# Kernel tuning notes

Hardware: AMD Instinct MI355X
Metric: run time of the kernel (lower is better)

Reference implementation:

```python
import jax, jax.numpy as jnp
import numpy as np

N = 100000   # nodes
E = 1600000  # edges
D = 128      # input_dim
H = 128      # hidden_dim
O = 64       # output_dim


def setup_inputs() -> dict:
    key = jax.random.key(0)
    ks = jax.random.split(key, 10)
    x = jax.random.normal(ks[0], (N, D), dtype=jnp.float32)
    edge_index = jax.random.randint(ks[1], (2, E), 0, N, dtype=jnp.int32)

    def glorot(k, fan_in, fan_out):
        lim = np.sqrt(6.0 / (fan_in + fan_out)).astype(np.float32)
        return jax.random.uniform(k, (fan_in, fan_out), jnp.float32, -lim, lim)

    return {
        "x": x,
        "edge_index": edge_index,
        "W0": glorot(ks[2], D, H), "b0": jnp.zeros((H,), jnp.float32),
        "W1": glorot(ks[3], H, H), "b1": jnp.zeros((H,), jnp.float32),
        "W2": glorot(ks[4], H, H), "b2": jnp.zeros((H,), jnp.float32),
        "W3": glorot(ks[5], H, O), "b3": jnp.zeros((O,), jnp.float32),
    }


def gcn_conv(x, src, dst, W, b):
    """PyG GCNConv: out = D^{-1/2} (A + I) D^{-1/2} (x W) + b."""
    n = x.shape[0]
    h = x @ W                                # [N, out]
    loop = jnp.arange(n, dtype=src.dtype)    # self loops
    s = jnp.concatenate([src, loop])
    d = jnp.concatenate([dst, loop])
    deg = jax.ops.segment_sum(jnp.ones_like(d, dtype=h.dtype), d, num_segments=n)
    dinv = jax.lax.rsqrt(jnp.maximum(deg, 1.0))  # deg >= 1 because of self loops
    norm = dinv[s] * dinv[d]                     # [E+N]
    out = jax.ops.segment_sum(h[s] * norm[:, None], d, num_segments=n)
    return out + b


def reference(x, edge_index, W0, b0, W1, b1, W2, b2, W3, b3):
    src, dst = edge_index[0], edge_index[1]
    # three GCNBlocks: GCNConv + ReLU (dropout disabled)
    h = jax.nn.relu(gcn_conv(x, src, dst, W0, b0))
    h = jax.nn.relu(gcn_conv(h, src, dst, W1, b1))
    h = jax.nn.relu(gcn_conv(h, src, dst, W2, b2))
    # final bare GCNConv -> output_dim (no activation)
    return gcn_conv(h, src, dst, W3, b3)
```

## Files before the change

kernel.cpp:

```cpp
#include <hip/hip_runtime.h>
#include <math.h>

#define NN 100000
#define NE 1600000
#define NB 391

typedef __attribute__((ext_vector_type(8))) short short8;
typedef __attribute__((ext_vector_type(4))) float f32x4;
union frag8 { short s[8]; short8 v; };

__device__ __forceinline__ void split_bf16(float a, short& hi, short& lo) {
    unsigned u = __float_as_uint(a);
    unsigned hb = u & 0xffff0000u;
    hi = (short)(hb >> 16);
    float r = a - __uint_as_float(hb);
    unsigned lu = __float_as_uint(r);
    lo = (short)((lu + 0x7fff + ((lu >> 16) & 1)) >> 16);
}

__global__ __launch_bounds__(256) void hist_k(const int* __restrict__ dst, int* __restrict__ hist, int e) {
    __shared__ int h[NB];
    int t = threadIdx.x;
    for (int i = t; i < NB; i += 256) h[i] = 0;
    __syncthreads();
    int base = blockIdx.x * 4096;
#pragma unroll
    for (int j = 0; j < 16; ++j) {
        int i = base + j * 256 + t;
        if (i < e) atomicAdd(&h[dst[i] >> 8], 1);
    }
    __syncthreads();
    for (int i = t; i < NB; i += 256) if (h[i]) atomicAdd(&hist[i], h[i]);
}

__global__ __launch_bounds__(512) void bktscan_k(const int* __restrict__ hist,
                                                 int* __restrict__ boff, int* __restrict__ bcur) {
    __shared__ int wsum[8];
    int t = threadIdx.x, lane = t & 63, wid = t >> 6;
    int v = (t < NB) ? hist[t] : 0;
    int inc = v;
#pragma unroll
    for (int off = 1; off < 64; off <<= 1) {
        int tt = __shfl_up(inc, off);
        if (lane >= off) inc += tt;
    }
    if (lane == 63) wsum[wid] = inc;
    __syncthreads();
    int woff = 0;
    for (int w = 0; w < wid; ++w) woff += wsum[w];
    int excl = inc - v + woff;
    if (t < NB) { boff[t] = excl; bcur[t] = excl; }
    if (t == NB - 1) boff[NB] = excl + v;
}

__global__ __launch_bounds__(256) void part2_k(const int* __restrict__ src, const int* __restrict__ dst,
                                               int* bcur, int2* __restrict__ pairs, int e) {
    __shared__ int lhist[NB];
    __shared__ int lbase[NB];
    int t = threadIdx.x;
    for (int i = t; i < NB; i += 256) lhist[i] = 0;
    __syncthreads();
    int e0 = blockIdx.x * 4096;
    int sreg[16], dreg[16];
#pragma unroll
    for (int j = 0; j < 16; ++j) {
        int i = e0 + j * 256 + t;
        if (i < e) {
            sreg[j] = src[i];
            dreg[j] = dst[i];
            atomicAdd(&lhist[dreg[j] >> 8], 1);
        } else dreg[j] = -1;
    }
    __syncthreads();
    for (int i = t; i < NB; i += 256) {
        int c = lhist[i];
        lbase[i] = c ? atomicAdd(&bcur[i], c) : 0;
        lhist[i] = 0;
    }
    __syncthreads();
#pragma unroll
    for (int j = 0; j < 16; ++j) {
        if (dreg[j] >= 0) {
            int b = dreg[j] >> 8;
            int pos = lbase[b] + atomicAdd(&lhist[b], 1);
            pairs[pos] = make_int2(sreg[j], dreg[j]);
        }
    }
}

__global__ __launch_bounds__(256) void csr_k(const int2* __restrict__ pairs, const int* __restrict__ boff,
                                             float* __restrict__ dinv, int* __restrict__ rowptr,
                                             int* __restrict__ csr_src, int n) {
    __shared__ int cnt[256];
    __shared__ int wsum[4];
    __shared__ int lcur[256];
    int b = blockIdx.x, t = threadIdx.x;
    cnt[t] = 0;
    __syncthreads();
    int e0 = boff[b], e1 = boff[b + 1];
    for (int e = e0 + t; e < e1; e += 256) atomicAdd(&cnt[pairs[e].y & 255], 1);
    __syncthreads();
    int c = cnt[t];
    int lane = t & 63, wid = t >> 6;
    int inc = c;
#pragma unroll
    for (int off = 1; off < 64; off <<= 1) {
        int tt = __shfl_up(inc, off);
        if (lane >= off) inc += tt;
    }
    if (lane == 63) wsum[wid] = inc;
    __syncthreads();
    int woff = 0;
    for (int w = 0; w < wid; ++w) woff += wsum[w];
    int excl = inc - c + woff + e0;
    int i = (b << 8) + t;
    if (i < n) {
        rowptr[i] = excl;
        dinv[i] = 1.0f / sqrtf((float)(c + 1));
    }
    if (b == NB - 1 && t == 255) rowptr[n] = e1;
    lcur[t] = excl;
    __syncthreads();
    for (int e = e0 + t; e < e1; e += 256) {
        int2 p = pairs[e];
        int pos = atomicAdd(&lcur[p.y & 255], 1);
        csr_src[pos] = p.x;
    }
}

__global__ __launch_bounds__(256) void convw_k(const float* __restrict__ W0, const float* __restrict__ W1,
                                               const float* __restrict__ W2, const float* __restrict__ W3,
                                               short* __restrict__ wt) {
    int gid = blockIdx.x * 256 + threadIdx.x;
    if (gid >= 57344) return;
    const float* W;
    int elem, Ncols, hi_base;
    if (gid < 49152) {
        int w = gid >> 14;
        elem = gid & 16383;
        Ncols = 128;
        W = (w == 0) ? W0 : (w == 1) ? W1 : W2;
        hi_base = w * 32768;
    } else {
        elem = gid - 49152;
        Ncols = 64;
        W = W3;
        hi_base = 98304;
    }
    int k = elem / Ncols, ncol = elem % Ncols;
    short hi, lo;
    split_bf16(W[elem], hi, lo);
    int dstidx = ncol * 128 + k;
    wt[hi_base + dstidx] = hi;
    wt[hi_base + Ncols * 128 + dstidx] = lo;
}

__global__ __launch_bounds__(256) void mfma_gemm_k(const float* __restrict__ A,
                                                   const short* __restrict__ wt_hi,
                                                   const short* __restrict__ wt_lo,
                                                   const float* __restrict__ dinv,
                                                   float* __restrict__ C, int n) {
    constexpr int NT = 8;
    const int tid = threadIdx.x;
    const int wid = tid >> 6, lane = tid & 63;
    const int arow = blockIdx.x * 64 + wid * 16 + (lane & 15);
    const int khalf = lane >> 4;

    f32x4 acc[NT];
#pragma unroll
    for (int nt = 0; nt < NT; ++nt) acc[nt] = (f32x4){0.f, 0.f, 0.f, 0.f};

#pragma unroll
    for (int kc = 0; kc < 4; ++kc) {
        const int k0 = kc * 32 + khalf * 8;
        float4 a0 = make_float4(0.f, 0.f, 0.f, 0.f), a1 = a0;
        if (arow < n) {
            a0 = *(const float4*)(A + (size_t)arow * 128 + k0);
            a1 = *(const float4*)(A + (size_t)arow * 128 + k0 + 4);
        }
        frag8 ahi, alo;
        float av[8] = {a0.x, a0.y, a0.z, a0.w, a1.x, a1.y, a1.z, a1.w};
#pragma unroll
        for (int j = 0; j < 8; ++j) split_bf16(av[j], ahi.s[j], alo.s[j]);

#pragma unroll
        for (int nt = 0; nt < NT; ++nt) {
            const size_t bidx = (size_t)(nt * 16 + (lane & 15)) * 128 + k0;
            short8 bhi = *(const short8*)(wt_hi + bidx);
            short8 blo = *(const short8*)(wt_lo + bidx);
            acc[nt] = __builtin_amdgcn_mfma_f32_16x16x32_bf16(alo.v, bhi, acc[nt], 0, 0, 0);
            acc[nt] = __builtin_amdgcn_mfma_f32_16x16x32_bf16(ahi.v, blo, acc[nt], 0, 0, 0);
            acc[nt] = __builtin_amdgcn_mfma_f32_16x16x32_bf16(ahi.v, bhi, acc[nt], 0, 0, 0);
        }
    }

    const int rbase = blockIdx.x * 64 + wid * 16 + khalf * 4;
    const int col = lane & 15;
    float dv[4];
#pragma unroll
    for (int r = 0; r < 4; ++r) dv[r] = (rbase + r < n) ? dinv[rbase + r] : 0.f;
#pragma unroll
    for (int nt = 0; nt < NT; ++nt) {
#pragma unroll
        for (int r = 0; r < 4; ++r) {
            int row = rbase + r;
            if (row < n) C[(size_t)row * 128 + nt * 16 + col] = acc[nt][r] * dv[r];
        }
    }
}

template<int HOUT>
__global__ __launch_bounds__(256) void fused_k(const float* __restrict__ tmp,
                                               const int* __restrict__ csr_src,
                                               const int* __restrict__ rowptr,
                                               const float* __restrict__ dinv,
                                               const float* __restrict__ bias,
                                               const short* __restrict__ wt_hi,
                                               const short* __restrict__ wt_lo,
                                               float* __restrict__ C) {
    constexpr int NT = HOUT / 32;
    __shared__ float As[32][132];
    const int t = threadIdx.x;
    const int row0 = blockIdx.x * 32;

    {
        const int l = t & 31;
        const int sub = t >> 5;
        float4 bb = *(const float4*)(bias + l * 4);
        int eptr[4], eend[4];
#pragma unroll
        for (int it = 0; it < 4; ++it) {
            int node = row0 + it * 8 + sub;
            eptr[it] = rowptr[node];
            eend[it] = rowptr[node + 1];
        }
        int pf = (eptr[0] + l < eend[0]) ? csr_src[eptr[0] + l] : 0;
#pragma unroll
        for (int it = 0; it < 4; ++it) {
            const int node = row0 + it * 8 + sub;
            const float dn = dinv[node];
            float4 acc = *(const float4*)(tmp + (size_t)node * 128 + l * 4);
            int myidx = pf;
            if (it < 3)
                pf = (eptr[it + 1] + l < eend[it + 1]) ? csr_src[eptr[it + 1] + l] : 0;
            int e = eptr[it];
            const int end = eend[it];
            while (e < end) {
                int m = end - e;
                if (m > 32) m = 32;
                int j = 0;
                for (; j + 4 <= m; j += 4) {
                    int s0 = __shfl(myidx, j, 32);
                    int s1 = __shfl(myidx, j + 1, 32);
                    int s2 = __shfl(myidx, j + 2, 32);
                    int s3 = __shfl(myidx, j + 3, 32);
                    float4 v0 = *(const float4*)(tmp + (size_t)s0 * 128 + l * 4);
                    float4 v1 = *(const float4*)(tmp + (size_t)s1 * 128 + l * 4);
                    float4 v2 = *(const float4*)(tmp + (size_t)s2 * 128 + l * 4);
                    float4 v3 = *(const float4*)(tmp + (size_t)s3 * 128 + l * 4);
                    acc.x += (v0.x + v1.x) + (v2.x + v3.x);
                    acc.y += (v0.y + v1.y) + (v2.y + v3.y);
                    acc.z += (v0.z + v1.z) + (v2.z + v3.z);
                    acc.w += (v0.w + v1.w) + (v2.w + v3.w);
                }
                for (; j < m; ++j) {
                    int s0 = __shfl(myidx, j, 32);
                    float4 v0 = *(const float4*)(tmp + (size_t)s0 * 128 + l * 4);
                    acc.x += v0.x; acc.y += v0.y; acc.z += v0.z; acc.w += v0.w;
                }
                e += m;
                if (e < end)
                    myidx = (e + l < end) ? csr_src[e + l] : 0;
            }
            acc.x = fmaxf(fmaf(acc.x, dn, bb.x), 0.f);
            acc.y = fmaxf(fmaf(acc.y, dn, bb.y), 0.f);
            acc.z = fmaxf(fmaf(acc.z, dn, bb.z), 0.f);
            acc.w = fmaxf(fmaf(acc.w, dn, bb.w), 0.f);
            *(float4*)&As[it * 8 + sub][l * 4] = acc;
        }
    }
    __syncthreads();

    const int wid = t >> 6, lane = t & 63;
    const int rt = wid & 1;
    const int cg = wid >> 1;
    const int arow_l = rt * 16 + (lane & 15);
    const int khalf = lane >> 4;

    f32x4 acc[NT];
#pragma unroll
    for (int nt = 0; nt < NT; ++nt) acc[nt] = (f32x4){0.f, 0.f, 0.f, 0.f};

#pragma unroll
    for (int kc = 0; kc < 4; ++kc) {
        const int k0 = kc * 32 + khalf * 8;
        float4 a0 = *(const float4*)&As[arow_l][k0];
        float4 a1 = *(const float4*)&As[arow_l][k0 + 4];
        frag8 ahi, alo;
        float av[8] = {a0.x, a0.y, a0.z, a0.w, a1.x, a1.y, a1.z, a1.w};
#pragma unroll
        for (int j = 0; j < 8; ++j) split_bf16(av[j], ahi.s[j], alo.s[j]);

#pragma unroll
        for (int nt = 0; nt < NT; ++nt) {
            const size_t bidx = (size_t)(cg * NT * 16 + nt * 16 + (lane & 15)) * 128 + k0;
            short8 bhi = *(const short8*)(wt_hi + bidx);
            short8 blo = *(const short8*)(wt_lo + bidx);
            acc[nt] = __builtin_amdgcn_mfma_f32_16x16x32_bf16(alo.v, bhi, acc[nt], 0, 0, 0);
            acc[nt] = __builtin_amdgcn_mfma_f32_16x16x32_bf16(ahi.v, blo, acc[nt], 0, 0, 0);
            acc[nt] = __builtin_amdgcn_mfma_f32_16x16x32_bf16(ahi.v, bhi, acc[nt], 0, 0, 0);
        }
    }

    const int rbase = row0 + rt * 16 + khalf * 4;
    const int col = lane & 15;
    float dv[4];
#pragma unroll
    for (int r = 0; r < 4; ++r) dv[r] = dinv[rbase + r];
#pragma unroll
    for (int nt = 0; nt < NT; ++nt) {
#pragma unroll
        for (int r = 0; r < 4; ++r) {
            C[(size_t)(rbase + r) * HOUT + cg * NT * 16 + nt * 16 + col] = acc[nt][r] * dv[r];
        }
    }
}

template<int HOUT>
__global__ __launch_bounds__(256) void agg2_k(const float* __restrict__ tmp,
                                              const int* __restrict__ csr_src,
                                              const int* __restrict__ rowptr,
                                              const float* __restrict__ dinv,
                                              const float* __restrict__ bias,
                                              float* __restrict__ out, int n) {
    constexpr int LPN = HOUT / 4;
    int gid = blockIdx.x * 256 + threadIdx.x;
    int node = gid / LPN, l = gid % LPN;
    if (node >= n) return;

    const float dn = dinv[node];
    float4 bb = *(const float4*)(bias + l * 4);
    float4 acc = *(const float4*)(tmp + (size_t)node * HOUT + l * 4);

    int e = rowptr[node];
    const int end = rowptr[node + 1];
    while (e < end) {
        int m = end - e;
        if (m > LPN) m = LPN;
        int myidx = (e + l < end) ? csr_src[e + l] : 0;
        int j = 0;
        for (; j + 4 <= m; j += 4) {
            int s0 = __shfl(myidx, j, LPN);
            int s1 = __shfl(myidx, j + 1, LPN);
            int s2 = __shfl(myidx, j + 2, LPN);
            int s3 = __shfl(myidx, j + 3, LPN);
            float4 v0 = *(const float4*)(tmp + (size_t)s0 * HOUT + l * 4);
            float4 v1 = *(const float4*)(tmp + (size_t)s1 * HOUT + l * 4);
            float4 v2 = *(const float4*)(tmp + (size_t)s2 * HOUT + l * 4);
            float4 v3 = *(const float4*)(tmp + (size_t)s3 * HOUT + l * 4);
            acc.x += (v0.x + v1.x) + (v2.x + v3.x);
            acc.y += (v0.y + v1.y) + (v2.y + v3.y);
            acc.z += (v0.z + v1.z) + (v2.z + v3.z);
            acc.w += (v0.w + v1.w) + (v2.w + v3.w);
        }
        for (; j < m; ++j) {
            int s0 = __shfl(myidx, j, LPN);
            float4 v0 = *(const float4*)(tmp + (size_t)s0 * HOUT + l * 4);
            acc.x += v0.x; acc.y += v0.y; acc.z += v0.z; acc.w += v0.w;
        }
        e += m;
    }
    float4 o;
    o.x = fmaf(acc.x, dn, bb.x);
    o.y = fmaf(acc.y, dn, bb.y);
    o.z = fmaf(acc.z, dn, bb.z);
    o.w = fmaf(acc.w, dn, bb.w);
    *(float4*)(out + (size_t)node * HOUT + l * 4) = o;
}

extern "C" void kernel_launch(void* const* d_in, const int* in_sizes, int n_in,
                              void* d_out, int out_size, void* d_ws, size_t ws_size,
                              hipStream_t stream) {
    const float* x    = (const float*)d_in[0];
    const int*   ei   = (const int*)d_in[1];
    const int*   srcp = ei;
    const int*   dstp = ei + NE;
    const float* W0 = (const float*)d_in[2]; const float* b0 = (const float*)d_in[3];
    const float* W1 = (const float*)d_in[4]; const float* b1 = (const float*)d_in[5];
    const float* W2 = (const float*)d_in[6]; const float* b2 = (const float*)d_in[7];
    const float* W3 = (const float*)d_in[8]; const float* b3 = (const float*)d_in[9];
    float* out = (float*)d_out;

    char* ws = (char*)d_ws;
    size_t off = 0;
    auto alloc = [&](size_t bytes) { void* p = ws + off; off = (off + bytes + 255) & ~(size_t)255; return p; };
    int*   hist    = (int*)alloc((size_t)NB * 4);
    int*   boff    = (int*)alloc((size_t)(NB + 1) * 4);
    int*   bcur    = (int*)alloc((size_t)NB * 4);
    float* dinv    = (float*)alloc((size_t)NN * 4);
    int*   rowptr  = (int*)alloc((size_t)(NN + 1) * 4);
    int*   csr_src = (int*)alloc((size_t)NE * 4);
    short* wt      = (short*)alloc((size_t)114688 * 2);
    float* bufA    = (float*)alloc((size_t)NN * 128 * 4);
    float* bufB    = (float*)alloc((size_t)NN * 128 * 4);
    int2*  pairs   = (int2*)bufA;

    const int nblk_e4k  = (NE + 4095) / 4096;
    const int nblk_g    = (NN + 63) / 64;
    const int nblk_f    = NN / 32;
    const int nblk_a64  = (int)(((size_t)NN * 16 + 255) / 256);

    hipMemsetAsync(hist, 0, (size_t)NB * 4, stream);
    hist_k<<<nblk_e4k, 256, 0, stream>>>(dstp, hist, NE);
    bktscan_k<<<1, 512, 0, stream>>>(hist, boff, bcur);
    part2_k<<<nblk_e4k, 256, 0, stream>>>(srcp, dstp, bcur, pairs, NE);
    csr_k<<<NB, 256, 0, stream>>>(pairs, boff, dinv, rowptr, csr_src, NN);
    convw_k<<<(57344 + 255) / 256, 256, 0, stream>>>(W0, W1, W2, W3, wt);

    const short* w0h = wt,          *w0l = wt + 16384;
    const short* w1h = wt + 32768,  *w1l = wt + 49152;
    const short* w2h = wt + 65536,  *w2l = wt + 81920;
    const short* w3h = wt + 98304,  *w3l = wt + 106496;

    mfma_gemm_k<<<nblk_g, 256, 0, stream>>>(x, w0h, w0l, dinv, bufB, NN);
    fused_k<128><<<nblk_f, 256, 0, stream>>>(bufB, csr_src, rowptr, dinv, b0, w1h, w1l, bufA);
    fused_k<128><<<nblk_f, 256, 0, stream>>>(bufA, csr_src, rowptr, dinv, b1, w2h, w2l, bufB);
    fused_k<64><<<nblk_f, 256, 0, stream>>>(bufB, csr_src, rowptr, dinv, b2, w3h, w3l, bufA);
    agg2_k<64><<<nblk_a64, 256, 0, stream>>>(bufA, csr_src, rowptr, dinv, b3, out, NN);
}
```

Before: 618.1 us.

## Replace histogram+scan CSR build with fixed-capacity bucket slots and row descriptors

Measured after the change: 604.8 us. 1.02x faster.

```diff
diff --git a/kernel.cpp b/kernel.cpp
--- a/kernel.cpp
+++ b/kernel.cpp
@@ -4,6 +4,7 @@
 #define NN 100000
 #define NE 1600000
 #define NB 391
+#define CAP 4608
 
 typedef __attribute__((ext_vector_type(8))) short short8;
 typedef __attribute__((ext_vector_type(4))) float f32x4;
@@ -18,41 +19,6 @@
     lo = (short)((lu + 0x7fff + ((lu >> 16) & 1)) >> 16);
 }
 
-__global__ __launch_bounds__(256) void hist_k(const int* __restrict__ dst, int* __restrict__ hist, int e) {
-    __shared__ int h[NB];
-    int t = threadIdx.x;
-    for (int i = t; i < NB; i += 256) h[i] = 0;
-    __syncthreads();
-    int base = blockIdx.x * 4096;
-#pragma unroll
-    for (int j = 0; j < 16; ++j) {
-        int i = base + j * 256 + t;
-        if (i < e) atomicAdd(&h[dst[i] >> 8], 1);
-    }
-    __syncthreads();
-    for (int i = t; i < NB; i += 256) if (h[i]) atomicAdd(&hist[i], h[i]);
-}
-
-__global__ __launch_bounds__(512) void bktscan_k(const int* __restrict__ hist,
-                                                 int* __restrict__ boff, int* __restrict__ bcur) {
-    __shared__ int wsum[8];
-    int t = threadIdx.x, lane = t & 63, wid = t >> 6;
-    int v = (t < NB) ? hist[t] : 0;
-    int inc = v;
-#pragma unroll
-    for (int off = 1; off < 64; off <<= 1) {
-        int tt = __shfl_up(inc, off);
-        if (lane >= off) inc += tt;
-    }
-    if (lane == 63) wsum[wid] = inc;
-    __syncthreads();
-    int woff = 0;
-    for (int w = 0; w < wid; ++w) woff += wsum[w];
-    int excl = inc - v + woff;
-    if (t < NB) { boff[t] = excl; bcur[t] = excl; }
-    if (t == NB - 1) boff[NB] = excl + v;
-}
-
 __global__ __launch_bounds__(256) void part2_k(const int* __restrict__ src, const int* __restrict__ dst,
                                                int* bcur, int2* __restrict__ pairs, int e) {
     __shared__ int lhist[NB];
@@ -74,7 +40,7 @@
     __syncthreads();
     for (int i = t; i < NB; i += 256) {
         int c = lhist[i];
-        lbase[i] = c ? atomicAdd(&bcur[i], c) : 0;
+        lbase[i] = c ? (i * CAP + atomicAdd(&bcur[i], c)) : 0;
         lhist[i] = 0;
     }
     __syncthreads();
@@ -88,17 +54,23 @@
     }
 }
 
-__global__ __launch_bounds__(256) void csr_k(const int2* __restrict__ pairs, const int* __restrict__ boff,
-                                             float* __restrict__ dinv, int* __restrict__ rowptr,
-                                             int* __restrict__ csr_src, int n) {
+__global__ __launch_bounds__(256) void csr2_k(const int2* __restrict__ pairs, const int* __restrict__ bcur,
+                                              float* __restrict__ dinv, int2* __restrict__ rowdesc,
+                                              int* __restrict__ csr_src, int n) {
+    __shared__ int2 lp[CAP];
     __shared__ int cnt[256];
     __shared__ int wsum[4];
     __shared__ int lcur[256];
     int b = blockIdx.x, t = threadIdx.x;
+    const int tot = bcur[b];
+    const int e0 = b * CAP;
     cnt[t] = 0;
     __syncthreads();
-    int e0 = boff[b], e1 = boff[b + 1];
-    for (int e = e0 + t; e < e1; e += 256) atomicAdd(&cnt[pairs[e].y & 255], 1);
+    for (int e = t; e < tot; e += 256) {
+        int2 p = pairs[e0 + e];
+        lp[e] = p;
+        atomicAdd(&cnt[p.y & 255], 1);
+    }
     __syncthreads();
     int c = cnt[t];
     int lane = t & 63, wid = t >> 6;
@@ -115,14 +87,13 @@
     int excl = inc - c + woff + e0;
     int i = (b << 8) + t;
     if (i < n) {
-        rowptr[i] = excl;
+        rowdesc[i] = make_int2(excl, c);
         dinv[i] = 1.0f / sqrtf((float)(c + 1));
     }
-    if (b == NB - 1 && t == 255) rowptr[n] = e1;
     lcur[t] = excl;
     __syncthreads();
-    for (int e = e0 + t; e < e1; e += 256) {
-        int2 p = pairs[e];
+    for (int e = t; e < tot; e += 256) {
+        int2 p = lp[e];
         int pos = atomicAdd(&lcur[p.y & 255], 1);
         csr_src[pos] = p.x;
     }
@@ -212,7 +183,7 @@
 template<int HOUT>
 __global__ __launch_bounds__(256) void fused_k(const float* __restrict__ tmp,
                                                const int* __restrict__ csr_src,
-                                               const int* __restrict__ rowptr,
+                                               const int2* __restrict__ rowdesc,
                                                const float* __restrict__ dinv,
                                                const float* __restrict__ bias,
                                                const short* __restrict__ wt_hi,
@@ -230,9 +201,9 @@
         int eptr[4], eend[4];
 #pragma unroll
         for (int it = 0; it < 4; ++it) {
-            int node = row0 + it * 8 + sub;
-            eptr[it] = rowptr[node];
-            eend[it] = rowptr[node + 1];
+            int2 rd = rowdesc[row0 + it * 8 + sub];
+            eptr[it] = rd.x;
+            eend[it] = rd.x + rd.y;
         }
         int pf = (eptr[0] + l < eend[0]) ? csr_src[eptr[0] + l] : 0;
 #pragma unroll
@@ -329,7 +300,7 @@
 template<int HOUT>
 __global__ __launch_bounds__(256) void agg2_k(const float* __restrict__ tmp,
                                               const int* __restrict__ csr_src,
-                                              const int* __restrict__ rowptr,
+                                              const int2* __restrict__ rowdesc,
                                               const float* __restrict__ dinv,
                                               const float* __restrict__ bias,
                                               float* __restrict__ out, int n) {
@@ -342,8 +313,9 @@
     float4 bb = *(const float4*)(bias + l * 4);
     float4 acc = *(const float4*)(tmp + (size_t)node * HOUT + l * 4);
 
-    int e = rowptr[node];
-    const int end = rowptr[node + 1];
+    int2 rd = rowdesc[node];
+    int e = rd.x;
+    const int end = rd.x + rd.y;
     while (e < end) {
         int m = end - e;
         if (m > LPN) m = LPN;
@@ -394,12 +366,10 @@
     char* ws = (char*)d_ws;
     size_t off = 0;
     auto alloc = [&](size_t bytes) { void* p = ws + off; off = (off + bytes + 255) & ~(size_t)255; return p; };
-    int*   hist    = (int*)alloc((size_t)NB * 4);
-    int*   boff    = (int*)alloc((size_t)(NB + 1) * 4);
     int*   bcur    = (int*)alloc((size_t)NB * 4);
     float* dinv    = (float*)alloc((size_t)NN * 4);
-    int*   rowptr  = (int*)alloc((size_t)(NN + 1) * 4);
-    int*   csr_src = (int*)alloc((size_t)NE * 4);
+    int2*  rowdesc = (int2*)alloc((size_t)NN * 8);
+    int*   csr_src = (int*)alloc((size_t)NB * CAP * 4);
     short* wt      = (short*)alloc((size_t)114688 * 2);
     float* bufA    = (float*)alloc((size_t)NN * 128 * 4);
     float* bufB    = (float*)alloc((size_t)NN * 128 * 4);
@@ -410,11 +380,9 @@
     const int nblk_f    = NN / 32;
     const int nblk_a64  = (int)(((size_t)NN * 16 + 255) / 256);
 
-    hipMemsetAsync(hist, 0, (size_t)NB * 4, stream);
-    hist_k<<<nblk_e4k, 256, 0, stream>>>(dstp, hist, NE);
-    bktscan_k<<<1, 512, 0, stream>>>(hist, boff, bcur);
+    hipMemsetAsync(bcur, 0, (size_t)NB * 4, stream);
     part2_k<<<nblk_e4k, 256, 0, stream>>>(srcp, dstp, bcur, pairs, NE);
-    csr_k<<<NB, 256, 0, stream>>>(pairs, boff, dinv, rowptr, csr_src, NN);
+    csr2_k<<<NB, 256, 0, stream>>>(pairs, bcur, dinv, rowdesc, csr_src, NN);
     convw_k<<<(57344 + 255) / 256, 256, 0, stream>>>(W0, W1, W2, W3, wt);
 
     const short* w0h = wt,          *w0l = wt + 16384;
@@ -423,8 +391,8 @@
     const short* w3h = wt + 98304,  *w3l = wt + 106496;
 
     mfma_gemm_k<<<nblk_g, 256, 0, stream>>>(x, w0h, w0l, dinv, bufB, NN);
-    fused_k<128><<<nblk_f, 256, 0, stream>>>(bufB, csr_src, rowptr, dinv, b0, w1h, w1l, bufA);
-    fused_k<128><<<nblk_f, 256, 0, stream>>>(bufA, csr_src, rowptr, dinv, b1, w2h, w2l, bufB);
-    fused_k<64><<<nblk_f, 256, 0, stream>>>(bufB, csr_src, rowptr, dinv, b2, w3h, w3l, bufA);
-    agg2_k<64><<<nblk_a64, 256, 0, stream>>>(bufA, csr_src, rowptr, dinv, b3, out, NN);
-}
+    fused_k<128><<<nblk_f, 256, 0, stream>>>(bufB, csr_src, rowdesc, dinv, b0, w1h, w1l, bufA);
+    fused_k<128><<<nblk_f, 256, 0, stream>>>(bufA, csr_src, rowdesc, dinv, b1, w2h, w2l, bufB);
+    fused_k<64><<<nblk_f, 256, 0, stream>>>(bufB, csr_src, rowdesc, dinv, b2, w3h, w3l, bufA);
+    agg2_k<64><<<nblk_a64, 256, 0, stream>>>(bufA, csr_src, rowdesc, dinv, b3, out, NN);
+}
```
